# Kernel optimization log

Hardware: AMD Instinct MI355X
Metric: run time of the kernel (lower is better)

Reference implementation:

```python
import jax, jax.numpy as jnp
import numpy as np

HEADS = 16
LN_EPS = 1e-6

def _layernorm(x, scale, bias):
    mu = jnp.mean(x, axis=-1, keepdims=True)
    var = jnp.mean(jnp.square(x - mu), axis=-1, keepdims=True)
    return (x - mu) * jax.lax.rsqrt(var + LN_EPS) * scale + bias

def setup_inputs() -> dict:
    key = jax.random.key(0)
    ks = jax.random.split(key, 5)
    B, L, D, F = 2, 2048, 1024, 4096
    s = lambda fan_in: 1.0 / np.sqrt(fan_in)
    return {
        'x': jax.random.normal(ks[0], (B, L, D), jnp.float32),
        'ln1_scale': jnp.ones((D,), jnp.float32),
        'ln1_bias': jnp.zeros((D,), jnp.float32),
        'w_qkv': jax.random.normal(ks[1], (D, 3 * D), jnp.float32) * s(D),
        'w_proj': jax.random.normal(ks[2], (D, D), jnp.float32) * s(D),
        'b_proj': jnp.zeros((D,), jnp.float32),
        'ln2_scale': jnp.ones((D,), jnp.float32),
        'ln2_bias': jnp.zeros((D,), jnp.float32),
        'w_mlp1': jax.random.normal(ks[3], (D, F), jnp.float32) * s(D),
        'b_mlp1': jnp.zeros((F,), jnp.float32),
        'w_mlp2': jax.random.normal(ks[4], (F, D), jnp.float32) * s(F),
        'b_mlp2': jnp.zeros((D,), jnp.float32),
    }

def reference(x, ln1_scale, ln1_bias, w_qkv, w_proj, b_proj,
              ln2_scale, ln2_bias, w_mlp1, b_mlp1, w_mlp2, b_mlp2):
    B, L, D = x.shape
    H = HEADS
    hd = D // H
    # pre-norm attention
    h = _layernorm(x, ln1_scale, ln1_bias)
    qkv = h @ w_qkv  # [B,L,3D]
    q, k, v = jnp.split(qkv, 3, axis=-1)
    q = q.reshape(B, L, H, hd).transpose(0, 2, 1, 3)  # [B,H,L,hd]
    k = k.reshape(B, L, H, hd).transpose(0, 2, 1, 3)
    v = v.reshape(B, L, H, hd).transpose(0, 2, 1, 3)
    scale = jnp.sqrt(jnp.float32(hd))
    scores = jnp.einsum('bhqd,bhkd->bhqk', q, k) / scale  # [B,H,L,L]
    attn = jax.nn.softmax(scores, axis=-1)
    out = jnp.einsum('bhqk,bhkd->bhqd', attn, v)  # [B,H,L,hd]
    out = out.transpose(0, 2, 1, 3).reshape(B, L, D)
    x = x + out @ w_proj + b_proj
    # pre-norm MLP
    h = _layernorm(x, ln2_scale, ln2_bias)
    m = jax.nn.gelu(h @ w_mlp1 + b_mlp1, approximate=True)
    return x + m @ w_mlp2 + b_mlp2
```

## Files before the change

kernel.cpp:

```cpp
#include <hip/hip_runtime.h>
#include <cstdint>
#include <cstddef>

typedef __bf16 bf16;
typedef __bf16 bf16x8 __attribute__((ext_vector_type(8)));
typedef float f32x4 __attribute__((ext_vector_type(4)));
typedef short short4v __attribute__((ext_vector_type(4)));

#define GLB_AS(p) ((const __attribute__((address_space(1))) unsigned*)(unsigned long long)(p))
#define LDS_AS(p) ((__attribute__((address_space(3))) unsigned*)(unsigned)(unsigned long long)(p))

__device__ __forceinline__ void g2l16(const void* g, void* l) {
  __builtin_amdgcn_global_load_lds(GLB_AS(g), LDS_AS(l), 16, 0, 0);
}

__device__ __forceinline__ short f2bf(float x) {
  bf16 h = (bf16)x;
  return __builtin_bit_cast(short, h);
}

extern "C" __device__ __attribute__((const)) float __ocml_native_exp2_f32(float);
__device__ __forceinline__ float fast_exp2(float x) {
  return __ocml_native_exp2_f32(x);
}

constexpr int MROWS = 4096;
constexpr size_t ATILE = (size_t)MROWS * 32;

#define QSCALE 0.18033688011112042f

__device__ __forceinline__ void transpose_body(
    const float* __restrict__ in, bf16* __restrict__ out, int K, int N,
    int bx, int by, float (*tile)[33], int tid)
{
  int tx = tid & 31, ty = tid >> 5;
  int n0 = bx * 32, k0 = by * 32;
  for (int i = ty; i < 32; i += 8)
    tile[i][tx] = in[(size_t)(k0 + i) * N + n0 + tx];
  __syncthreads();
  bf16* obase = out + (size_t)(k0 >> 5) * N * 32;
  for (int i = ty; i < 32; i += 8)
    obase[(size_t)(n0 + i) * 32 + tx] = (bf16)tile[tx][i];
}

__device__ __forceinline__ void ln_body(
    const float* __restrict__ x, const float* __restrict__ sc,
    const float* __restrict__ bi, bf16* __restrict__ out,
    int row, float* wsum, float* wsq, int tid)
{
  const float* xr = x + (size_t)row * 1024;
  int c = tid * 4;
  float4 xv = *(const float4*)(xr + c);
  float s = xv.x + xv.y + xv.z + xv.w;
  float q = xv.x * xv.x + xv.y * xv.y + xv.z * xv.z + xv.w * xv.w;
#pragma unroll
  for (int off = 1; off < 64; off <<= 1) {
    s += __shfl_xor(s, off);
    q += __shfl_xor(q, off);
  }
  int wv = tid >> 6;
  if ((tid & 63) == 0) { wsum[wv] = s; wsq[wv] = q; }
  __syncthreads();
  s = wsum[0] + wsum[1] + wsum[2] + wsum[3];
  q = wsq[0] + wsq[1] + wsq[2] + wsq[3];
  float mean = s * (1.f / 1024.f);
  float var = q * (1.f / 1024.f) - mean * mean;
  float rstd = rsqrtf(var + 1e-6f);
  float4 scv = *(const float4*)(sc + c);
  float4 biv = *(const float4*)(bi + c);
  bf16* o = out + (size_t)(c >> 5) * ATILE + (size_t)row * 32 + (c & 31);
  o[0] = (bf16)((xv.x - mean) * rstd * scv.x + biv.x);
  o[1] = (bf16)((xv.y - mean) * rstd * scv.y + biv.y);
  o[2] = (bf16)((xv.z - mean) * rstd * scv.z + biv.z);
  o[3] = (bf16)((xv.w - mean) * rstd * scv.w + biv.w);
}

__global__ __launch_bounds__(256) void prep_kernel(
    const float* __restrict__ wqkv, const float* __restrict__ wproj,
    const float* __restrict__ wmlp1, const float* __restrict__ wmlp2,
    bf16* __restrict__ wqkv_t, bf16* __restrict__ wproj_t,
    bf16* __restrict__ wmlp1_t, bf16* __restrict__ wmlp2_t,
    const float* __restrict__ x, const float* __restrict__ ln1s,
    const float* __restrict__ ln1b, bf16* __restrict__ hbuf)
{
  __shared__ float tile[32][33];
  __shared__ float wsum[4], wsq[4];
  int bid = blockIdx.x, tid = threadIdx.x;
  if (bid < 3072)
    transpose_body(wqkv, wqkv_t, 1024, 3072, bid % 96, bid / 96, tile, tid);
  else if (bid < 4096) {
    int i = bid - 3072;
    transpose_body(wproj, wproj_t, 1024, 1024, i % 32, i / 32, tile, tid);
  } else if (bid < 8192) {
    int i = bid - 4096;
    transpose_body(wmlp1, wmlp1_t, 1024, 4096, i % 128, i / 128, tile, tid);
  } else if (bid < 12288) {
    int i = bid - 8192;
    transpose_body(wmlp2, wmlp2_t, 4096, 1024, i % 32, i / 32, tile, tid);
  } else {
    ln_body(x, ln1s, ln1b, hbuf, bid - 12288, wsum, wsq, tid);
  }
}

__global__ __launch_bounds__(256) void ln_kernel(
    const float* __restrict__ x, const float* __restrict__ sc,
    const float* __restrict__ bi, bf16* __restrict__ out)
{
  __shared__ float wsum[4], wsq[4];
  ln_body(x, sc, bi, out, blockIdx.x, wsum, wsq, threadIdx.x);
}

template <int MT, int NT, int EPI>
__global__ __launch_bounds__(256) void gemm_tt(
    const bf16* __restrict__ A, const bf16* __restrict__ Bt,
    int N, int K,
    const float* __restrict__ bias, const float* __restrict__ resid,
    float* __restrict__ outf, bf16* __restrict__ ob0,
    bf16* __restrict__ ob1, bf16* __restrict__ ob2)
{
  constexpr int TM = MT * 32, TN = NT * 32;
  __shared__ __align__(16) bf16 As[2][TM * 32];
  __shared__ __align__(16) bf16 Bs[2][TN * 32];
  const int tid = threadIdx.x, lane = tid & 63, wave = tid >> 6;
  const int wm = wave >> 1, wn = wave & 1;
  const int quad = lane >> 4, l16 = lane & 15;

  int flat = blockIdx.x + gridDim.x * blockIdx.y;
  int xcd = flat & 7, rr = flat >> 3;
  int npx = gridDim.x >> 3;
  int bn = xcd * npx + (rr % npx);
  int bm = rr / npx;

  const size_t astride = ATILE;
  const size_t bstride = (size_t)N * 32;
  const bf16* Abase = A + (size_t)bm * TM * 32 + (size_t)lane * 8;
  const bf16* Bbase = Bt + (size_t)bn * TN * 32 + (size_t)lane * 8;

  f32x4 acc[MT][NT] = {};
  const int KT = K >> 5;

  auto stage = [&](int buf, int kt) {
    const bf16* Ab = Abase + (size_t)kt * astride;
    const bf16* Bb = Bbase + (size_t)kt * bstride;
#pragma unroll
    for (int i = 0; i < MT / 2; i++)
      g2l16(Ab + (wave + 4 * i) * 512, &As[buf][(wave + 4 * i) * 512]);
#pragma unroll
    for (int i = 0; i < NT / 2; i++)
      g2l16(Bb + (wave + 4 * i) * 512, &Bs[buf][(wave + 4 * i) * 512]);
  };

  stage(0, 0);
  int buf = 0;
  for (int kt = 0; kt < KT; kt++) {
    __syncthreads();
    if (kt + 1 < KT) stage(buf ^ 1, kt + 1);
    bf16x8 af[MT], bfr[NT];
#pragma unroll
    for (int mt = 0; mt < MT; mt++)
      af[mt] = *(const bf16x8*)&As[buf][(wm * MT * 16 + mt * 16 + l16) * 32 + quad * 8];
#pragma unroll
    for (int nt = 0; nt < NT; nt++)
      bfr[nt] = *(const bf16x8*)&Bs[buf][(wn * NT * 16 + nt * 16 + l16) * 32 + quad * 8];
#pragma unroll
    for (int mt = 0; mt < MT; mt++)
#pragma unroll
      for (int nt = 0; nt < NT; nt++)
        acc[mt][nt] = __builtin_amdgcn_mfma_f32_16x16x32_bf16(af[mt], bfr[nt], acc[mt][nt], 0, 0, 0);
    buf ^= 1;
  }

#pragma unroll
  for (int mt = 0; mt < MT; mt++) {
#pragma unroll
    for (int nt = 0; nt < NT; nt++) {
      int row0 = bm * TM + wm * MT * 16 + mt * 16 + quad * 4;
      int col = bn * TN + wn * NT * 16 + nt * 16 + l16;
      if (EPI == 0) {
        int b = row0 >> 11, l = row0 & 2047;
        int which = col >> 10, d = col & 1023;
        int hh = d >> 6, hdi = d & 63;
        size_t bh = (size_t)(b * 16 + hh);
        if (which == 0) {
#pragma unroll
          for (int r = 0; r < 4; r++)
            ob0[(bh * 2048 + l + r) * 64 + hdi] = (bf16)(acc[mt][nt][r] * QSCALE);
        } else if (which == 1) {
#pragma unroll
          for (int r = 0; r < 4; r++)
            ob1[(bh * 2048 + l + r) * 64 + hdi] = (bf16)acc[mt][nt][r];
        } else {
          short4v v4;
#pragma unroll
          for (int r = 0; r < 4; r++) v4[r] = f2bf(acc[mt][nt][r]);
          *(short4v*)&ob2[(bh * 64 + hdi) * 2048 + l] = v4;
        }
      } else {
#pragma unroll
        for (int r = 0; r < 4; r++) {
          int row = row0 + r;
          float v = acc[mt][nt][r];
          if (EPI == 1) {
            size_t idx = (size_t)row * N + col;
            outf[idx] = v + bias[col] + resid[idx];
          } else {
            float t = v + bias[col];
            float u = t + 0.044715f * t * t * t;
            float g = 0.5f * t * (1.f + tanhf(0.7978845608028654f * u));
            ob0[(size_t)(col >> 5) * ATILE + (size_t)row * 32 + (col & 31)] = (bf16)g;
          }
        }
      }
    }
  }
}

__global__ __launch_bounds__(256, 2) void flash_attn(
    const bf16* __restrict__ Q, const bf16* __restrict__ Kg,
    const bf16* __restrict__ Vg, bf16* __restrict__ O)
{
  __shared__ __align__(16) bf16 Ks[128 * 72];
  __shared__ __align__(16) bf16 Vs[64 * 136];
  const int tid = threadIdx.x, lane = tid & 63, wave = tid >> 6;
  const int quad = lane >> 4, l16 = lane & 15;
  const int qt = blockIdx.x, bh = blockIdx.y;
  const int b = bh >> 4, h = bh & 15;

  const bf16* qg = Q + ((size_t)bh * 2048 + qt * 128) * 64;
  const bf16* kg = Kg + (size_t)bh * 2048 * 64;
  const bf16* vg = Vg + (size_t)bh * 64 * 2048;

  bf16x8 qf[2][2];
#pragma unroll
  for (int s = 0; s < 2; s++)
#pragma unroll
    for (int kk = 0; kk < 2; kk++)
      qf[s][kk] = *(const bf16x8*)&qg[(size_t)(wave * 32 + s * 16 + l16) * 64 + kk * 32 + quad * 8];

  f32x4 oacc[2][4] = {};
  float lrow[2] = {0.f, 0.f};

  for (int kt = 0; kt < 16; kt++) {
    __syncthreads();
#pragma unroll
    for (int i = 0; i < 4; i++) {
      int t = tid + i * 256;
      *(bf16x8*)&Ks[(t >> 3) * 72 + (t & 7) * 8] =
          *(const bf16x8*)&kg[((size_t)kt * 128 + (t >> 3)) * 64 + (t & 7) * 8];
      *(bf16x8*)&Vs[(t >> 4) * 136 + (t & 15) * 8] =
          *(const bf16x8*)&vg[(size_t)(t >> 4) * 2048 + kt * 128 + (t & 15) * 8];
    }
    __syncthreads();

    f32x4 sacc[2][8] = {};
#pragma unroll
    for (int kk = 0; kk < 2; kk++) {
#pragma unroll
      for (int ct = 0; ct < 8; ct++) {
        bf16x8 kf = *(const bf16x8*)&Ks[(ct * 16 + l16) * 72 + kk * 32 + quad * 8];
        sacc[0][ct] = __builtin_amdgcn_mfma_f32_16x16x32_bf16(kf, qf[0][kk], sacc[0][ct], 0, 0, 0);
        sacc[1][ct] = __builtin_amdgcn_mfma_f32_16x16x32_bf16(kf, qf[1][kk], sacc[1][ct], 0, 0, 0);
      }
    }

    short4v pf[2][8];
#pragma unroll
    for (int s = 0; s < 2; s++) {
      float sum = 0.f;
#pragma unroll
      for (int ct = 0; ct < 8; ct++) {
#pragma unroll
        for (int r = 0; r < 4; r++) {
          float p = fast_exp2(sacc[s][ct][r]);
          sum += p;
          pf[s][ct][r] = f2bf(p);
        }
      }
      sum += __shfl_xor(sum, 16);
      sum += __shfl_xor(sum, 32);
      lrow[s] += sum;
    }

#pragma unroll
    for (int ot = 0; ot < 4; ot++) {
#pragma unroll
      for (int ct = 0; ct < 8; ct++) {
        short4v vf = *(const short4v*)&Vs[(ot * 16 + l16) * 136 + ct * 16 + quad * 4];
        oacc[0][ot] = __builtin_amdgcn_mfma_f32_16x16x16bf16_1k(vf, pf[0][ct], oacc[0][ot], 0, 0, 0);
        oacc[1][ot] = __builtin_amdgcn_mfma_f32_16x16x16bf16_1k(vf, pf[1][ct], oacc[1][ot], 0, 0, 0);
      }
    }
  }

#pragma unroll
  for (int s = 0; s < 2; s++) {
    float inv = 1.f / lrow[s];
    int qrow = qt * 128 + wave * 32 + s * 16 + l16;
    size_t grow = (size_t)b * 2048 + qrow;
#pragma unroll
    for (int ot = 0; ot < 4; ot++) {
      int col = h * 64 + ot * 16 + quad * 4;
      short4v o4;
#pragma unroll
      for (int r = 0; r < 4; r++) o4[r] = f2bf(oacc[s][ot][r] * inv);
      *(short4v*)&O[(size_t)(col >> 5) * ATILE + grow * 32 + (col & 31)] = o4;
    }
  }
}

extern "C" void kernel_launch(void* const* d_in, const int* in_sizes, int n_in,
                              void* d_out, int out_size, void* d_ws, size_t ws_size,
                              hipStream_t stream)
{
  const float* x     = (const float*)d_in[0];
  const float* ln1s  = (const float*)d_in[1];
  const float* ln1b  = (const float*)d_in[2];
  const float* wqkv  = (const float*)d_in[3];
  const float* wproj = (const float*)d_in[4];
  const float* bproj = (const float*)d_in[5];
  const float* ln2s  = (const float*)d_in[6];
  const float* ln2b  = (const float*)d_in[7];
  const float* wmlp1 = (const float*)d_in[8];
  const float* bmlp1 = (const float*)d_in[9];
  const float* wmlp2 = (const float*)d_in[10];
  const float* bmlp2 = (const float*)d_in[11];
  float* out = (float*)d_out;

  char* ws = (char*)d_ws;
  bf16* wqkv_t  = (bf16*)(ws + 0);
  bf16* wproj_t = (bf16*)(ws + 6291456);
  bf16* wmlp1_t = (bf16*)(ws + 8388608);
  bf16* wmlp2_t = (bf16*)(ws + 16777216);
  bf16* hbuf    = (bf16*)(ws + 25165824);
  bf16* qb      = (bf16*)(ws + 33554432);
  bf16* kb      = (bf16*)(ws + 41943040);
  bf16* vb      = (bf16*)(ws + 50331648);
  bf16* aout    = (bf16*)(ws + 58720256);
  bf16* mbuf    = (bf16*)(ws + 33554432);

  prep_kernel<<<16384, 256, 0, stream>>>(wqkv, wproj, wmlp1, wmlp2,
                                         wqkv_t, wproj_t, wmlp1_t, wmlp2_t,
                                         x, ln1s, ln1b, hbuf);
  gemm_tt<4, 4, 0><<<dim3(24, 32), 256, 0, stream>>>(hbuf, wqkv_t, 3072, 1024,
                                                     nullptr, nullptr, nullptr, qb, kb, vb);
  flash_attn<<<dim3(16, 32), 256, 0, stream>>>(qb, kb, vb, aout);
  gemm_tt<2, 4, 1><<<dim3(8, 64), 256, 0, stream>>>(aout, wproj_t, 1024, 1024,
                                                    bproj, x, out, nullptr, nullptr, nullptr);
  ln_kernel<<<4096, 256, 0, stream>>>(out, ln2s, ln2b, hbuf);
  gemm_tt<4, 4, 2><<<dim3(32, 32), 256, 0, stream>>>(hbuf, wmlp1_t, 4096, 1024,
                                                     bmlp1, nullptr, nullptr, mbuf, nullptr, nullptr);
  gemm_tt<2, 4, 1><<<dim3(8, 64), 256, 0, stream>>>(mbuf, wmlp2_t, 1024, 4096,
                                                    bmlp2, out, out, nullptr, nullptr, nullptr);
}
```

Measured before the change: 357.1 us.

## Register-prefetch K/V tiles in flash attention and use fast GELU tanh

The flash attention loop now loads the next K/V tile from global memory into registers while the current tile is being computed, overlapping global latency with MFMA work. The softmax row-sum shuffles are moved out of the loop to a single reduction at the end. Probabilities are packed to bf16 in pairs. GELU's tanhf is replaced with an exp2/reciprocal approximation. These changes add register pressure from prefetch buffers and slightly reduce tanh accuracy.

```diff
diff --git a/kernel.cpp b/kernel.cpp
--- a/kernel.cpp
+++ b/kernel.cpp
@@ -1,4 +1,5 @@
 #include <hip/hip_runtime.h>
+#include <hip/hip_bf16.h>
 #include <cstdint>
 #include <cstddef>
 
@@ -6,6 +7,7 @@
 typedef __bf16 bf16x8 __attribute__((ext_vector_type(8)));
 typedef float f32x4 __attribute__((ext_vector_type(4)));
 typedef short short4v __attribute__((ext_vector_type(4)));
+typedef unsigned uint2v __attribute__((ext_vector_type(2)));
 
 #define GLB_AS(p) ((const __attribute__((address_space(1))) unsigned*)(unsigned long long)(p))
 #define LDS_AS(p) ((__attribute__((address_space(3))) unsigned*)(unsigned)(unsigned long long)(p))
@@ -19,9 +21,21 @@
   return __builtin_bit_cast(short, h);
 }
 
+__device__ __forceinline__ unsigned pk_bf16(float a, float b) {
+  __hip_bfloat162 h = __float22bfloat162_rn(float2{a, b});
+  unsigned u;
+  __builtin_memcpy(&u, &h, 4);
+  return u;
+}
+
 extern "C" __device__ __attribute__((const)) float __ocml_native_exp2_f32(float);
+extern "C" __device__ __attribute__((const)) float __ocml_native_recip_f32(float);
 __device__ __forceinline__ float fast_exp2(float x) {
   return __ocml_native_exp2_f32(x);
+}
+__device__ __forceinline__ float fast_tanh(float a) {
+  float e = __ocml_native_exp2_f32(a * 2.8853900817779268f);
+  return 1.f - 2.f * __ocml_native_recip_f32(e + 1.f);
 }
 
 constexpr int MROWS = 4096;
@@ -205,8 +219,8 @@
             outf[idx] = v + bias[col] + resid[idx];
           } else {
             float t = v + bias[col];
-            float u = t + 0.044715f * t * t * t;
-            float g = 0.5f * t * (1.f + tanhf(0.7978845608028654f * u));
+            float a = 0.7978845608028654f * t * (1.f + 0.044715f * t * t);
+            float g = 0.5f * t * (1.f + fast_tanh(a));
             ob0[(size_t)(col >> 5) * ATILE + (size_t)row * 32 + (col & 31)] = (bf16)g;
           }
         }
@@ -240,17 +254,31 @@
   f32x4 oacc[2][4] = {};
   float lrow[2] = {0.f, 0.f};
 
+  bf16x8 kreg[4], vreg[4];
+#pragma unroll
+  for (int i = 0; i < 4; i++) {
+    int t = tid + i * 256;
+    kreg[i] = *(const bf16x8*)&kg[(size_t)(t >> 3) * 64 + (t & 7) * 8];
+    vreg[i] = *(const bf16x8*)&vg[(size_t)(t >> 4) * 2048 + (t & 15) * 8];
+  }
+
   for (int kt = 0; kt < 16; kt++) {
     __syncthreads();
 #pragma unroll
     for (int i = 0; i < 4; i++) {
       int t = tid + i * 256;
-      *(bf16x8*)&Ks[(t >> 3) * 72 + (t & 7) * 8] =
-          *(const bf16x8*)&kg[((size_t)kt * 128 + (t >> 3)) * 64 + (t & 7) * 8];
-      *(bf16x8*)&Vs[(t >> 4) * 136 + (t & 15) * 8] =
-          *(const bf16x8*)&vg[(size_t)(t >> 4) * 2048 + kt * 128 + (t & 15) * 8];
+      *(bf16x8*)&Ks[(t >> 3) * 72 + (t & 7) * 8] = kreg[i];
+      *(bf16x8*)&Vs[(t >> 4) * 136 + (t & 15) * 8] = vreg[i];
     }
     __syncthreads();
+    if (kt < 15) {
+#pragma unroll
+      for (int i = 0; i < 4; i++) {
+        int t = tid + i * 256;
+        kreg[i] = *(const bf16x8*)&kg[((size_t)(kt + 1) * 128 + (t >> 3)) * 64 + (t & 7) * 8];
+        vreg[i] = *(const bf16x8*)&vg[(size_t)(t >> 4) * 2048 + (kt + 1) * 128 + (t & 15) * 8];
+      }
+    }
 
     f32x4 sacc[2][8] = {};
 #pragma unroll
@@ -269,15 +297,16 @@
       float sum = 0.f;
 #pragma unroll
       for (int ct = 0; ct < 8; ct++) {
-#pragma unroll
-        for (int r = 0; r < 4; r++) {
-          float p = fast_exp2(sacc[s][ct][r]);
-          sum += p;
-          pf[s][ct][r] = f2bf(p);
-        }
-      }
-      sum += __shfl_xor(sum, 16);
-      sum += __shfl_xor(sum, 32);
+        float p0 = fast_exp2(sacc[s][ct][0]);
+        float p1 = fast_exp2(sacc[s][ct][1]);
+        float p2 = fast_exp2(sacc[s][ct][2]);
+        float p3 = fast_exp2(sacc[s][ct][3]);
+        sum += (p0 + p1) + (p2 + p3);
+        uint2v u;
+        u[0] = pk_bf16(p0, p1);
+        u[1] = pk_bf16(p2, p3);
+        pf[s][ct] = __builtin_bit_cast(short4v, u);
+      }
       lrow[s] += sum;
     }
 
@@ -294,7 +323,10 @@
 
 #pragma unroll
   for (int s = 0; s < 2; s++) {
-    float inv = 1.f / lrow[s];
+    float l = lrow[s];
+    l += __shfl_xor(l, 16);
+    l += __shfl_xor(l, 32);
+    float inv = 1.f / l;
     int qrow = qt * 128 + wave * 32 + s * 16 + l16;
     size_t grow = (size_t)b * 2048 + qrow;
 #pragma unroll
```

Measured after the change: 340.9 us. 4.5% less time.
